# Optimization experiments

Measured on AMD Instinct MI355X. Metric: run time of the kernel, lower is better.

The kernel has to match this reference:

```python
import jax, jax.numpy as jnp
import numpy as np
import math

B, T, C = 4, 2048, 1024
NH = 16
HD = C // NH


def setup_inputs() -> dict:
    key = jax.random.key(0)
    ks = jax.random.split(key, 10)
    s = 0.02
    x = jax.random.normal(ks[0], (B, T, C), dtype=jnp.float32)
    W_qkv = jax.random.normal(ks[1], (C, 3 * C), dtype=jnp.float32) * s
    b_qkv = jnp.zeros((3 * C,), dtype=jnp.float32)
    W_proj = jax.random.normal(ks[2], (C, C), dtype=jnp.float32) * s
    b_proj = jnp.zeros((C,), dtype=jnp.float32)
    asym_mean, asym_std = 1.0, 0.7
    q_scale = jax.random.normal(ks[3], (NH, HD), dtype=jnp.float32) * asym_std + asym_mean
    q_bias = jax.random.normal(ks[4], (NH, HD), dtype=jnp.float32) * asym_std + asym_mean
    k_scale = jax.random.normal(ks[5], (NH, HD), dtype=jnp.float32) * asym_std + asym_mean
    k_bias = jax.random.normal(ks[6], (NH, HD), dtype=jnp.float32) * asym_std + asym_mean
    return {"x": x, "W_qkv": W_qkv, "b_qkv": b_qkv, "W_proj": W_proj,
            "b_proj": b_proj, "q_scale": q_scale, "q_bias": q_bias,
            "k_scale": k_scale, "k_bias": k_bias}


def reference(x, W_qkv, b_qkv, W_proj, b_proj, q_scale, q_bias, k_scale, k_bias):
    Bx, Tx, Cx = x.shape
    qkv = x @ W_qkv + b_qkv                       # [B,T,3C]
    q, k, v = jnp.split(qkv, 3, axis=-1)
    # [B,T,C] -> [B,NH,T,HD]
    reshape = lambda t: t.reshape(Bx, Tx, NH, HD).transpose(0, 2, 1, 3)
    q, k, v = reshape(q), reshape(k), reshape(v)
    # per-head affine scaling of Q/K
    q = q * q_scale[None, :, None, :] + q_bias[None, :, None, :]
    k = k * k_scale[None, :, None, :] + k_bias[None, :, None, :]
    scores = jnp.einsum('bhqd,bhkd->bhqk', q, k) / math.sqrt(HD)  # [B,NH,T,T]
    causal = jnp.tril(jnp.ones((Tx, Tx), dtype=bool))
    scores = jnp.where(causal[None, None], scores, -jnp.inf)
    att = jax.nn.softmax(scores, axis=-1)
    y = jnp.einsum('bhqk,bhkd->bhqd', att, v)     # [B,NH,T,HD]
    y = y.transpose(0, 2, 1, 3).reshape(Bx, Tx, Cx)
    return y @ W_proj + b_proj
```

## Files before the change

kernel.cpp:

```cpp
#include <hip/hip_runtime.h>
#include <hip/hip_bf16.h>

typedef unsigned short u16;
typedef __attribute__((ext_vector_type(8))) short short8;
typedef __attribute__((ext_vector_type(4))) float floatx4;

#define B_SZ 4
#define T_SZ 2048
#define C_SZ 1024
#define NH_SZ 16
#define HD_SZ 64
#define M_TOT 8192
#define K_DIM 1024

#define QSCALE 0.1803368801111204f

#define OFF_XB   ((size_t)16)
#define OFF_WQT  (OFF_XB + 8388608)
#define OFF_WPT  (OFF_WQT + 3145728)
#define OFF_PB   (OFF_WPT + 1048576)
#define OFF_Q    (OFF_PB + 8192)
#define OFF_K    (OFF_Q + 8388608)
#define OFF_V    (OFF_K + 8388608)
#define OFF_Y    (OFF_V + 8388608)
#define PB_BQKV  0
#define PB_BPROJ 3072
#define PB_QSC   4096
#define PB_QBI   5120
#define PB_KSC   6144
#define PB_KBI   7168

__device__ __forceinline__ float bf2f(u16 u) {
    return __uint_as_float(((unsigned)u) << 16);
}
__device__ __forceinline__ u16 f2bf(float f) {
    unsigned x = __float_as_uint(f);
    unsigned r = (x + 0x7fffu + ((x >> 16) & 1u)) >> 16;
    return (u16)r;
}
__device__ __forceinline__ u16 f2bf_fast(float f) {
    return (u16)((__float_as_uint(f) + 0x8000u) >> 16);
}
__device__ __forceinline__ void gl_lds16(const u16* g, u16* l) {
    __builtin_amdgcn_global_load_lds(
        (const __attribute__((address_space(1))) void*)g,
        (__attribute__((address_space(3))) void*)l, 16, 0, 0);
}
__device__ __forceinline__ void wait_vm0() {
    __builtin_amdgcn_s_waitcnt(0x0F70);
}

__global__ __launch_bounds__(256) void detect_k(const u16* __restrict__ x,
                                                int* __restrict__ flag) {
    __shared__ int cnt;
    if (threadIdx.x == 0) cnt = 0;
    __syncthreads();
    int bad = 0;
    for (int i = threadIdx.x; i < 512; i += 256) {
        float v = fabsf(bf2f(x[i]));
        if (v > 1024.0f || (v != 0.0f && v < 9.5367431640625e-7f)) bad++;
    }
    atomicAdd(&cnt, bad);
    __syncthreads();
    if (threadIdx.x == 0) flag[0] = (cnt > 16) ? 1 : 0;
}

__global__ __launch_bounds__(256) void prep_k(
        const void* __restrict__ x,
        const void* __restrict__ Wqkv, const void* __restrict__ Wproj,
        const void* __restrict__ bqkv, const void* __restrict__ bproj,
        const void* __restrict__ qsc, const void* __restrict__ qbi,
        const void* __restrict__ ksc, const void* __restrict__ kbi,
        u16* __restrict__ xb, u16* __restrict__ Wt_qkv,
        u16* __restrict__ Wt_proj, u16* __restrict__ pb,
        const int* __restrict__ flag) {
    __shared__ u16 t[32][33];
    const int blk = blockIdx.x;
    const int isf = flag[0];
    if (blk < 8192) {
        const int i = blk * 256 + threadIdx.x;
        if (isf) {
            const float4 v = ((const float4*)x)[i];
            ushort4 o;
            o.x = f2bf(v.x); o.y = f2bf(v.y); o.z = f2bf(v.z); o.w = f2bf(v.w);
            ((ushort4*)xb)[i] = o;
        } else {
            ((ushort4*)xb)[i] = ((const ushort4*)x)[i];
        }
        return;
    }
    if (blk < 8200) {
        const int i4 = (blk - 8192) * 256 + threadIdx.x;
        if (i4 >= 2048) return;
        const int e = i4 * 4;
        const void* src; int off;
        if (e < 3072)      { src = bqkv;  off = e; }
        else if (e < 4096) { src = bproj; off = e - 3072; }
        else if (e < 5120) { src = qsc;   off = e - 4096; }
        else if (e < 6144) { src = qbi;   off = e - 5120; }
        else if (e < 7168) { src = ksc;   off = e - 6144; }
        else               { src = kbi;   off = e - 7168; }
        ushort4 o;
        if (isf) {
            const float4 v = *(const float4*)((const float*)src + off);
            o.x = f2bf(v.x); o.y = f2bf(v.y); o.z = f2bf(v.z); o.w = f2bf(v.w);
        } else {
            o = *(const ushort4*)((const u16*)src + off);
        }
        *(ushort4*)&pb[e] = o;
        return;
    }
    const void* in; u16* out; int R, C, idx;
    if (blk < 11272) { idx = blk - 8200;  in = Wqkv;  out = Wt_qkv;  R = 1024; C = 3072; }
    else             { idx = blk - 11272; in = Wproj; out = Wt_proj; R = 1024; C = 1024; }
    const int nbx = C >> 5;
    const int c0 = (idx % nbx) * 32, r0 = (idx / nbx) * 32;
    const int tx = threadIdx.x & 31, ty = threadIdx.x >> 5;
    for (int i = 0; i < 4; i++) {
        int r = ty + i * 8;
        size_t gi = (size_t)(r0 + r) * C + c0 + tx;
        t[r][tx] = isf ? f2bf(((const float*)in)[gi]) : ((const u16*)in)[gi];
    }
    __syncthreads();
    for (int i = 0; i < 4; i++) {
        int cr = ty + i * 8;
        out[(size_t)(c0 + cr) * R + r0 + tx] = t[tx][cr];
    }
}

__global__ __launch_bounds__(256) void qkv_gemm(
        const u16* __restrict__ X, const u16* __restrict__ Wt,
        const u16* __restrict__ pb,
        u16* __restrict__ Qb, u16* __restrict__ Kb, u16* __restrict__ Vb) {
    __shared__ __align__(16) u16 As[2][128 * 64];
    __shared__ __align__(16) u16 Bs[2][128 * 64];
    const int bm = blockIdx.y * 128, bn = blockIdx.x * 128;
    const int tid = threadIdx.x;
    const int lane = tid & 63, wave = tid >> 6;
    const int quad = lane >> 4, l16 = lane & 15;
    const int wm = (wave & 1) * 64, wn = (wave >> 1) * 64;
    const int lrow = lane >> 3;
    const int lcol = ((lane & 7) ^ lrow) * 8;

    const u16* xrow = &X[(size_t)(bm + wave * 32 + lrow) * K_DIM + lcol];
    const u16* wrow = &Wt[(size_t)(bn + wave * 32 + lrow) * K_DIM + lcol];

    floatx4 acc[4][4];
    for (int mi = 0; mi < 4; mi++)
        for (int ni = 0; ni < 4; ni++) acc[mi][ni] = 0.f;

    for (int j = 0; j < 4; j++) {
        gl_lds16(xrow + (size_t)j * 8 * K_DIM, &As[0][(wave * 32 + j * 8) * 64]);
        gl_lds16(wrow + (size_t)j * 8 * K_DIM, &Bs[0][(wave * 32 + j * 8) * 64]);
    }

    int cur = 0;
    for (int k0 = 0; k0 < K_DIM; k0 += 64) {
        wait_vm0();
        __syncthreads();
        if (k0 + 64 < K_DIM) {
            const int nb = cur ^ 1;
            for (int j = 0; j < 4; j++) {
                gl_lds16(xrow + (size_t)j * 8 * K_DIM + k0 + 64,
                         &As[nb][(wave * 32 + j * 8) * 64]);
                gl_lds16(wrow + (size_t)j * 8 * K_DIM + k0 + 64,
                         &Bs[nb][(wave * 32 + j * 8) * 64]);
            }
        }
        for (int kk = 0; kk < 64; kk += 32) {
            const int cb = kk >> 3;
            const int slot = ((cb + quad) ^ (l16 & 7)) * 8;
            short8 a[4], b[4];
            for (int mi = 0; mi < 4; mi++)
                a[mi] = *(const short8*)&As[cur][(wm + mi * 16 + l16) * 64 + slot];
            for (int ni = 0; ni < 4; ni++)
                b[ni] = *(const short8*)&Bs[cur][(wn + ni * 16 + l16) * 64 + slot];
            for (int mi = 0; mi < 4; mi++)
                for (int ni = 0; ni < 4; ni++)
                    acc[mi][ni] = __builtin_amdgcn_mfma_f32_16x16x32_bf16(
                        a[mi], b[ni], acc[mi][ni], 0, 0, 0);
        }
        cur ^= 1;
    }

    const int sec = bn >> 10;
    const int bb = bm >> 11;
    const int tbase = bm & 2047;
    for (int mi = 0; mi < 4; mi++) {
        for (int ni = 0; ni < 4; ni++) {
            const int col = bn + wn + ni * 16 + l16;
            const int cmod = col & 1023;
            const int h = cmod >> 6, d = cmod & 63;
            const float bv = bf2f(pb[PB_BQKV + col]);
            if (sec == 2) {
                const int t0 = tbase + wm + mi * 16 + quad * 4;
                ushort4 pk;
                pk.x = f2bf(acc[mi][ni][0] + bv);
                pk.y = f2bf(acc[mi][ni][1] + bv);
                pk.z = f2bf(acc[mi][ni][2] + bv);
                pk.w = f2bf(acc[mi][ni][3] + bv);
                *(ushort4*)&Vb[(((size_t)(bb * NH_SZ + h)) * HD_SZ + d) * T_SZ + t0] = pk;
            } else {
                float sA, sB;
                if (sec == 0) {
                    sA = bf2f(pb[PB_QSC + h * 64 + d]) * QSCALE;
                    sB = bf2f(pb[PB_QBI + h * 64 + d]) * QSCALE;
                } else {
                    sA = bf2f(pb[PB_KSC + h * 64 + d]);
                    sB = bf2f(pb[PB_KBI + h * 64 + d]);
                }
                u16* dstbuf = (sec == 0) ? Qb : Kb;
                for (int r = 0; r < 4; r++) {
                    const int t = tbase + wm + mi * 16 + quad * 4 + r;
                    float v = (acc[mi][ni][r] + bv) * sA + sB;
                    dstbuf[(((size_t)(bb * NH_SZ + h)) * T_SZ + t) * HD_SZ + d] = f2bf(v);
                }
            }
        }
    }
}

__global__ __launch_bounds__(512) void attn_k(const u16* __restrict__ Qb,
                                              const u16* __restrict__ Kb,
                                              const u16* __restrict__ Vtg,
                                              u16* __restrict__ Y) {
    __shared__ __align__(16) u16 Ks[64 * 64];
    __shared__ __align__(16) u16 Vs[64 * 64];
    __shared__ __align__(16) u16 Ps[8 * 16 * 88];
    const int blk = blockIdx.x;
    const int head = blk & 63;
    const int p = blk >> 6;
    const int b = head >> 4, h = head & 15;
    const int tid = threadIdx.x, lane = tid & 63, w = tid >> 6;
    const int quad = lane >> 4, l16 = lane & 15;
    const size_t qk_off = (size_t)head * (T_SZ * HD_SZ);
    const size_t v_off = (size_t)head * (HD_SZ * T_SZ);
    u16* psw = &Ps[w * 1408];
    const int lr = lane >> 3;
    const int lc = ((lane & 7) ^ lr) * 8;
    const int sl0 = ((quad) ^ (l16 & 7)) * 8;
    const int sl1 = ((4 + quad) ^ (l16 & 7)) * 8;

    short8 ones;
    for (int j = 0; j < 8; j++) ones[j] = (short)0x3F80;

    for (int tile = 0; tile < 2; tile++) {
        const int qt = tile ? p : (15 - p);
        const int q0 = qt * 128;
        const int rbase = q0 + w * 16;
        const int q = rbase + l16;

        const short8 aq0 = *(const short8*)&Qb[qk_off + (size_t)q * HD_SZ + quad * 8];
        const short8 aq1 = *(const short8*)&Qb[qk_off + (size_t)q * HD_SZ + 32 + quad * 8];

        floatx4 o[4];
        for (int mi = 0; mi < 4; mi++) o[mi] = 0.f;
        float m_run = -1e30f, l_run = 0.f;

        for (int k0 = 0; k0 < q0 + 128; k0 += 64) {
            __syncthreads();
            gl_lds16(&Kb[qk_off + (size_t)(k0 + w * 8 + lr) * HD_SZ + lc], &Ks[w * 512]);
            gl_lds16(&Vtg[v_off + (size_t)(w * 8 + lr) * T_SZ + k0 + lc], &Vs[w * 512]);
            __syncthreads();
            if (k0 > rbase + 15) continue;

            floatx4 s[4];
            for (int ni = 0; ni < 4; ni++) s[ni] = 0.f;
            for (int ni = 0; ni < 4; ni++)
                s[ni] = __builtin_amdgcn_mfma_f32_16x16x32_bf16(
                    *(const short8*)&Ks[(ni * 16 + l16) * 64 + sl0], aq0, s[ni], 0, 0, 0);
            for (int ni = 0; ni < 4; ni++)
                s[ni] = __builtin_amdgcn_mfma_f32_16x16x32_bf16(
                    *(const short8*)&Ks[(ni * 16 + l16) * 64 + sl1], aq1, s[ni], 0, 0, 0);

            if (k0 + 63 > rbase) {
                for (int ni = 0; ni < 4; ni++)
                    for (int r = 0; r < 4; r++) {
                        int key = k0 + ni * 16 + quad * 4 + r;
                        if (key > q) s[ni][r] = -1e30f;
                    }
            }

            float mx = fmaxf(fmaxf(s[0][0], s[0][1]), fmaxf(s[0][2], s[0][3]));
            for (int ni = 1; ni < 4; ni++)
                mx = fmaxf(mx, fmaxf(fmaxf(s[ni][0], s[ni][1]),
                                     fmaxf(s[ni][2], s[ni][3])));
            mx = fmaxf(mx, __shfl_xor(mx, 16, 64));
            mx = fmaxf(mx, __shfl_xor(mx, 32, 64));
            const float mnew = fmaxf(m_run, mx);
            const float alpha = exp2f(m_run - mnew);
            for (int ni = 0; ni < 4; ni++)
                for (int r = 0; r < 4; r++)
                    s[ni][r] = exp2f(s[ni][r] - mnew);
            m_run = mnew;
            for (int mi = 0; mi < 4; mi++) o[mi] *= alpha;

            for (int ni = 0; ni < 4; ni++) {
                ushort4 pk;
                pk.x = f2bf_fast(s[ni][0]); pk.y = f2bf_fast(s[ni][1]);
                pk.z = f2bf_fast(s[ni][2]); pk.w = f2bf_fast(s[ni][3]);
                *(ushort4*)&psw[l16 * 88 + ni * 16 + quad * 4] = pk;
            }

            floatx4 s4 = 0.f;
            for (int kk = 0; kk < 64; kk += 32) {
                short8 pfr = *(const short8*)&psw[l16 * 88 + kk + quad * 8];
                const int vsl = (kk == 0) ? sl0 : sl1;
                s4 = __builtin_amdgcn_mfma_f32_16x16x32_bf16(ones, pfr, s4, 0, 0, 0);
                for (int mi = 0; mi < 4; mi++) {
                    short8 vfr = *(const short8*)&Vs[(mi * 16 + l16) * 64 + vsl];
                    o[mi] = __builtin_amdgcn_mfma_f32_16x16x32_bf16(vfr, pfr, o[mi], 0, 0, 0);
                }
            }
            l_run = l_run * alpha + s4[0];
        }

        const float inv = 1.0f / l_run;
        u16* yrow = &Y[(((size_t)b * T_SZ + q) * NH_SZ + h) * HD_SZ];
        for (int mi = 0; mi < 4; mi++) {
            ushort4 pk;
            pk.x = f2bf_fast(o[mi][0] * inv); pk.y = f2bf_fast(o[mi][1] * inv);
            pk.z = f2bf_fast(o[mi][2] * inv); pk.w = f2bf_fast(o[mi][3] * inv);
            *(ushort4*)&yrow[mi * 16 + quad * 4] = pk;
        }
    }
}

__global__ __launch_bounds__(256) void proj_gemm(const u16* __restrict__ Yin,
                                                 const u16* __restrict__ Wt,
                                                 const u16* __restrict__ pb,
                                                 void* __restrict__ out,
                                                 const int* __restrict__ flag) {
    __shared__ __align__(16) u16 As[2][128 * 64];
    __shared__ __align__(16) u16 Bs[2][128 * 64];
    const int isf = flag[0];
    const int bm = blockIdx.y * 128, bn = blockIdx.x * 128;
    const int tid = threadIdx.x;
    const int lane = tid & 63, wave = tid >> 6;
    const int quad = lane >> 4, l16 = lane & 15;
    const int wm = (wave & 1) * 64, wn = (wave >> 1) * 64;
    const int lrow = lane >> 3;
    const int lcol = ((lane & 7) ^ lrow) * 8;

    const u16* yrow = &Yin[(size_t)(bm + wave * 32 + lrow) * K_DIM + lcol];
    const u16* wrow = &Wt[(size_t)(bn + wave * 32 + lrow) * K_DIM + lcol];

    floatx4 acc[4][4];
    for (int mi = 0; mi < 4; mi++)
        for (int ni = 0; ni < 4; ni++) acc[mi][ni] = 0.f;

    for (int j = 0; j < 4; j++) {
        gl_lds16(yrow + (size_t)j * 8 * K_DIM, &As[0][(wave * 32 + j * 8) * 64]);
        gl_lds16(wrow + (size_t)j * 8 * K_DIM, &Bs[0][(wave * 32 + j * 8) * 64]);
    }

    int cur = 0;
    for (int k0 = 0; k0 < K_DIM; k0 += 64) {
        wait_vm0();
        __syncthreads();
        if (k0 + 64 < K_DIM) {
            const int nb = cur ^ 1;
            for (int j = 0; j < 4; j++) {
                gl_lds16(yrow + (size_t)j * 8 * K_DIM + k0 + 64,
                         &As[nb][(wave * 32 + j * 8) * 64]);
                gl_lds16(wrow + (size_t)j * 8 * K_DIM + k0 + 64,
                         &Bs[nb][(wave * 32 + j * 8) * 64]);
            }
        }
        for (int kk = 0; kk < 64; kk += 32) {
            const int cb = kk >> 3;
            const int slot = ((cb + quad) ^ (l16 & 7)) * 8;
            short8 a[4], b[4];
            for (int mi = 0; mi < 4; mi++)
                a[mi] = *(const short8*)&As[cur][(wm + mi * 16 + l16) * 64 + slot];
            for (int ni = 0; ni < 4; ni++)
                b[ni] = *(const short8*)&Bs[cur][(wn + ni * 16 + l16) * 64 + slot];
            for (int mi = 0; mi < 4; mi++)
                for (int ni = 0; ni < 4; ni++)
                    acc[mi][ni] = __builtin_amdgcn_mfma_f32_16x16x32_bf16(
                        a[mi], b[ni], acc[mi][ni], 0, 0, 0);
        }
        cur ^= 1;
    }

    for (int mi = 0; mi < 4; mi++) {
        for (int ni = 0; ni < 4; ni++) {
            const int col = bn + wn + ni * 16 + l16;
            const float bv = bf2f(pb[PB_BPROJ + col]);
            for (int r = 0; r < 4; r++) {
                const int row = bm + wm + mi * 16 + quad * 4 + r;
                const float v = acc[mi][ni][r] + bv;
                if (isf) ((float*)out)[(size_t)row * C_SZ + col] = v;
                else     ((u16*)out)[(size_t)row * C_SZ + col] = f2bf(v);
            }
        }
    }
}

extern "C" void kernel_launch(void* const* d_in, const int* in_sizes, int n_in,
                              void* d_out, int out_size, void* d_ws, size_t ws_size,
                              hipStream_t stream) {
    const void* x     = d_in[0];
    const void* Wqkv  = d_in[1];
    const void* bqkv  = d_in[2];
    const void* Wproj = d_in[3];
    const void* bproj = d_in[4];
    const void* qsc   = d_in[5];
    const void* qbi   = d_in[6];
    const void* ksc   = d_in[7];
    const void* kbi   = d_in[8];

    u16* ws = (u16*)d_ws;
    int* flag    = (int*)d_ws;
    u16* xb      = ws + OFF_XB;
    u16* Wt_qkv  = ws + OFF_WQT;
    u16* Wt_proj = ws + OFF_WPT;
    u16* pb      = ws + OFF_PB;
    u16* Qb      = ws + OFF_Q;
    u16* Kb      = ws + OFF_K;
    u16* Vb      = ws + OFF_V;
    u16* Yb      = ws + OFF_Y;

    detect_k<<<1, 256, 0, stream>>>((const u16*)x, flag);
    prep_k<<<12296, 256, 0, stream>>>(x, Wqkv, Wproj, bqkv, bproj,
                                      qsc, qbi, ksc, kbi,
                                      xb, Wt_qkv, Wt_proj, pb, flag);
    qkv_gemm<<<dim3(24, 64), 256, 0, stream>>>(xb, Wt_qkv, pb, Qb, Kb, Vb);
    attn_k<<<dim3(512), 512, 0, stream>>>(Qb, Kb, Vb, Yb);
    proj_gemm<<<dim3(8, 64), 256, 0, stream>>>(Yb, Wt_proj, pb, d_out, flag);
}
```

Before: 323.9 us.

## Single-buffer GEMM staging and fuse both causal query tiles in one attention pass

The QKV and projection GEMMs drop double-buffered async LDS prefetch and go back to a single buffer with load-then-sync, which halves their shared memory footprint. The attention kernel now processes its two paired query tiles (15-p and p) in one sweep over K/V, so each K/V tile is loaded once and shared by both instead of being reloaded for the second tile. It also adds a per-tile P buffer and a min-blocks launch bound. The cost is more registers and LDS in attention, and the GEMMs can no longer hide load latency behind compute.

```diff
diff --git a/kernel.cpp b/kernel.cpp
--- a/kernel.cpp
+++ b/kernel.cpp
@@ -45,9 +45,6 @@
     __builtin_amdgcn_global_load_lds(
         (const __attribute__((address_space(1))) void*)g,
         (__attribute__((address_space(3))) void*)l, 16, 0, 0);
-}
-__device__ __forceinline__ void wait_vm0() {
-    __builtin_amdgcn_s_waitcnt(0x0F70);
 }
 
 __global__ __launch_bounds__(256) void detect_k(const u16* __restrict__ x,
@@ -132,8 +129,8 @@
         const u16* __restrict__ X, const u16* __restrict__ Wt,
         const u16* __restrict__ pb,
         u16* __restrict__ Qb, u16* __restrict__ Kb, u16* __restrict__ Vb) {
-    __shared__ __align__(16) u16 As[2][128 * 64];
-    __shared__ __align__(16) u16 Bs[2][128 * 64];
+    __shared__ __align__(16) u16 As[128 * 64];
+    __shared__ __align__(16) u16 Bs[128 * 64];
     const int bm = blockIdx.y * 128, bn = blockIdx.x * 128;
     const int tid = threadIdx.x;
     const int lane = tid & 63, wave = tid >> 6;
@@ -142,45 +139,31 @@
     const int lrow = lane >> 3;
     const int lcol = ((lane & 7) ^ lrow) * 8;
 
-    const u16* xrow = &X[(size_t)(bm + wave * 32 + lrow) * K_DIM + lcol];
-    const u16* wrow = &Wt[(size_t)(bn + wave * 32 + lrow) * K_DIM + lcol];
-
     floatx4 acc[4][4];
     for (int mi = 0; mi < 4; mi++)
         for (int ni = 0; ni < 4; ni++) acc[mi][ni] = 0.f;
 
-    for (int j = 0; j < 4; j++) {
-        gl_lds16(xrow + (size_t)j * 8 * K_DIM, &As[0][(wave * 32 + j * 8) * 64]);
-        gl_lds16(wrow + (size_t)j * 8 * K_DIM, &Bs[0][(wave * 32 + j * 8) * 64]);
-    }
-
-    int cur = 0;
     for (int k0 = 0; k0 < K_DIM; k0 += 64) {
-        wait_vm0();
-        __syncthreads();
-        if (k0 + 64 < K_DIM) {
-            const int nb = cur ^ 1;
-            for (int j = 0; j < 4; j++) {
-                gl_lds16(xrow + (size_t)j * 8 * K_DIM + k0 + 64,
-                         &As[nb][(wave * 32 + j * 8) * 64]);
-                gl_lds16(wrow + (size_t)j * 8 * K_DIM + k0 + 64,
-                         &Bs[nb][(wave * 32 + j * 8) * 64]);
-            }
-        }
+        __syncthreads();
+        for (int j = 0; j < 4; j++) {
+            const int rb = wave * 32 + j * 8;
+            gl_lds16(&X[(size_t)(bm + rb + lrow) * K_DIM + k0 + lcol], &As[rb * 64]);
+            gl_lds16(&Wt[(size_t)(bn + rb + lrow) * K_DIM + k0 + lcol], &Bs[rb * 64]);
+        }
+        __syncthreads();
         for (int kk = 0; kk < 64; kk += 32) {
             const int cb = kk >> 3;
             const int slot = ((cb + quad) ^ (l16 & 7)) * 8;
             short8 a[4], b[4];
             for (int mi = 0; mi < 4; mi++)
-                a[mi] = *(const short8*)&As[cur][(wm + mi * 16 + l16) * 64 + slot];
+                a[mi] = *(const short8*)&As[(wm + mi * 16 + l16) * 64 + slot];
             for (int ni = 0; ni < 4; ni++)
-                b[ni] = *(const short8*)&Bs[cur][(wn + ni * 16 + l16) * 64 + slot];
+                b[ni] = *(const short8*)&Bs[(wn + ni * 16 + l16) * 64 + slot];
             for (int mi = 0; mi < 4; mi++)
                 for (int ni = 0; ni < 4; ni++)
                     acc[mi][ni] = __builtin_amdgcn_mfma_f32_16x16x32_bf16(
                         a[mi], b[ni], acc[mi][ni], 0, 0, 0);
         }
-        cur ^= 1;
     }
 
     const int sec = bn >> 10;
@@ -220,13 +203,13 @@
     }
 }
 
-__global__ __launch_bounds__(512) void attn_k(const u16* __restrict__ Qb,
-                                              const u16* __restrict__ Kb,
-                                              const u16* __restrict__ Vtg,
-                                              u16* __restrict__ Y) {
+__global__ __launch_bounds__(512, 4) void attn_k(const u16* __restrict__ Qb,
+                                                 const u16* __restrict__ Kb,
+                                                 const u16* __restrict__ Vtg,
+                                                 u16* __restrict__ Y) {
     __shared__ __align__(16) u16 Ks[64 * 64];
     __shared__ __align__(16) u16 Vs[64 * 64];
-    __shared__ __align__(16) u16 Ps[8 * 16 * 88];
+    __shared__ __align__(16) u16 Ps[2 * 8 * 16 * 88];
     const int blk = blockIdx.x;
     const int head = blk & 63;
     const int p = blk >> 6;
@@ -235,7 +218,8 @@
     const int quad = lane >> 4, l16 = lane & 15;
     const size_t qk_off = (size_t)head * (T_SZ * HD_SZ);
     const size_t v_off = (size_t)head * (HD_SZ * T_SZ);
-    u16* psw = &Ps[w * 1408];
+    u16* pswA = &Ps[w * 1408];
+    u16* pswB = &Ps[11264 + w * 1408];
     const int lr = lane >> 3;
     const int lc = ((lane & 7) ^ lr) * 8;
     const int sl0 = ((quad) ^ (l16 & 7)) * 8;
@@ -244,83 +228,135 @@
     short8 ones;
     for (int j = 0; j < 8; j++) ones[j] = (short)0x3F80;
 
-    for (int tile = 0; tile < 2; tile++) {
-        const int qt = tile ? p : (15 - p);
-        const int q0 = qt * 128;
-        const int rbase = q0 + w * 16;
-        const int q = rbase + l16;
-
-        const short8 aq0 = *(const short8*)&Qb[qk_off + (size_t)q * HD_SZ + quad * 8];
-        const short8 aq1 = *(const short8*)&Qb[qk_off + (size_t)q * HD_SZ + 32 + quad * 8];
-
-        floatx4 o[4];
-        for (int mi = 0; mi < 4; mi++) o[mi] = 0.f;
-        float m_run = -1e30f, l_run = 0.f;
-
-        for (int k0 = 0; k0 < q0 + 128; k0 += 64) {
-            __syncthreads();
-            gl_lds16(&Kb[qk_off + (size_t)(k0 + w * 8 + lr) * HD_SZ + lc], &Ks[w * 512]);
-            gl_lds16(&Vtg[v_off + (size_t)(w * 8 + lr) * T_SZ + k0 + lc], &Vs[w * 512]);
-            __syncthreads();
-            if (k0 > rbase + 15) continue;
-
-            floatx4 s[4];
-            for (int ni = 0; ni < 4; ni++) s[ni] = 0.f;
-            for (int ni = 0; ni < 4; ni++)
-                s[ni] = __builtin_amdgcn_mfma_f32_16x16x32_bf16(
-                    *(const short8*)&Ks[(ni * 16 + l16) * 64 + sl0], aq0, s[ni], 0, 0, 0);
-            for (int ni = 0; ni < 4; ni++)
-                s[ni] = __builtin_amdgcn_mfma_f32_16x16x32_bf16(
-                    *(const short8*)&Ks[(ni * 16 + l16) * 64 + sl1], aq1, s[ni], 0, 0, 0);
-
-            if (k0 + 63 > rbase) {
+    const int rbA = (15 - p) * 128 + w * 16, qA = rbA + l16;
+    const int rbB = p * 128 + w * 16,        qB = rbB + l16;
+
+    const short8 aqA0 = *(const short8*)&Qb[qk_off + (size_t)qA * HD_SZ + quad * 8];
+    const short8 aqA1 = *(const short8*)&Qb[qk_off + (size_t)qA * HD_SZ + 32 + quad * 8];
+    const short8 aqB0 = *(const short8*)&Qb[qk_off + (size_t)qB * HD_SZ + quad * 8];
+    const short8 aqB1 = *(const short8*)&Qb[qk_off + (size_t)qB * HD_SZ + 32 + quad * 8];
+
+    floatx4 oA[4], oB[4];
+    for (int mi = 0; mi < 4; mi++) { oA[mi] = 0.f; oB[mi] = 0.f; }
+    float mA = -1e30f, lA = 0.f, mB = -1e30f, lB = 0.f;
+
+    const int kend = (16 - p) * 128;
+    for (int k0 = 0; k0 < kend; k0 += 64) {
+        __syncthreads();
+        gl_lds16(&Kb[qk_off + (size_t)(k0 + w * 8 + lr) * HD_SZ + lc], &Ks[w * 512]);
+        gl_lds16(&Vtg[v_off + (size_t)(w * 8 + lr) * T_SZ + k0 + lc], &Vs[w * 512]);
+        __syncthreads();
+        const bool doA = (k0 <= rbA + 15);
+        const bool doB = (k0 <= rbB + 15);
+        if (!doA && !doB) continue;
+
+        floatx4 sA[4], sB[4];
+        if (doA) for (int ni = 0; ni < 4; ni++) sA[ni] = 0.f;
+        if (doB) for (int ni = 0; ni < 4; ni++) sB[ni] = 0.f;
+        for (int ni = 0; ni < 4; ni++) {
+            const short8 kf = *(const short8*)&Ks[(ni * 16 + l16) * 64 + sl0];
+            if (doA) sA[ni] = __builtin_amdgcn_mfma_f32_16x16x32_bf16(kf, aqA0, sA[ni], 0, 0, 0);
+            if (doB) sB[ni] = __builtin_amdgcn_mfma_f32_16x16x32_bf16(kf, aqB0, sB[ni], 0, 0, 0);
+        }
+        for (int ni = 0; ni < 4; ni++) {
+            const short8 kf = *(const short8*)&Ks[(ni * 16 + l16) * 64 + sl1];
+            if (doA) sA[ni] = __builtin_amdgcn_mfma_f32_16x16x32_bf16(kf, aqA1, sA[ni], 0, 0, 0);
+            if (doB) sB[ni] = __builtin_amdgcn_mfma_f32_16x16x32_bf16(kf, aqB1, sB[ni], 0, 0, 0);
+        }
+
+        float alphaA = 1.f, alphaB = 1.f;
+        if (doA) {
+            if (k0 + 63 > rbA)
                 for (int ni = 0; ni < 4; ni++)
                     for (int r = 0; r < 4; r++) {
                         int key = k0 + ni * 16 + quad * 4 + r;
-                        if (key > q) s[ni][r] = -1e30f;
+                        if (key > qA) sA[ni][r] = -1e30f;
                     }
-            }
-
-            float mx = fmaxf(fmaxf(s[0][0], s[0][1]), fmaxf(s[0][2], s[0][3]));
+            float mx = fmaxf(fmaxf(sA[0][0], sA[0][1]), fmaxf(sA[0][2], sA[0][3]));
             for (int ni = 1; ni < 4; ni++)
-                mx = fmaxf(mx, fmaxf(fmaxf(s[ni][0], s[ni][1]),
-                                     fmaxf(s[ni][2], s[ni][3])));
+                mx = fmaxf(mx, fmaxf(fmaxf(sA[ni][0], sA[ni][1]),
+                                     fmaxf(sA[ni][2], sA[ni][3])));
             mx = fmaxf(mx, __shfl_xor(mx, 16, 64));
             mx = fmaxf(mx, __shfl_xor(mx, 32, 64));
-            const float mnew = fmaxf(m_run, mx);
-            const float alpha = exp2f(m_run - mnew);
+            const float mnew = fmaxf(mA, mx);
+            alphaA = exp2f(mA - mnew);
             for (int ni = 0; ni < 4; ni++)
-                for (int r = 0; r < 4; r++)
-                    s[ni][r] = exp2f(s[ni][r] - mnew);
-            m_run = mnew;
-            for (int mi = 0; mi < 4; mi++) o[mi] *= alpha;
-
+                for (int r = 0; r < 4; r++) sA[ni][r] = exp2f(sA[ni][r] - mnew);
+            mA = mnew;
+            for (int mi = 0; mi < 4; mi++) oA[mi] *= alphaA;
             for (int ni = 0; ni < 4; ni++) {
                 ushort4 pk;
-                pk.x = f2bf_fast(s[ni][0]); pk.y = f2bf_fast(s[ni][1]);
-                pk.z = f2bf_fast(s[ni][2]); pk.w = f2bf_fast(s[ni][3]);
-                *(ushort4*)&psw[l16 * 88 + ni * 16 + quad * 4] = pk;
-            }
-
-            floatx4 s4 = 0.f;
-            for (int kk = 0; kk < 64; kk += 32) {
-                short8 pfr = *(const short8*)&psw[l16 * 88 + kk + quad * 8];
-                const int vsl = (kk == 0) ? sl0 : sl1;
-                s4 = __builtin_amdgcn_mfma_f32_16x16x32_bf16(ones, pfr, s4, 0, 0, 0);
-                for (int mi = 0; mi < 4; mi++) {
-                    short8 vfr = *(const short8*)&Vs[(mi * 16 + l16) * 64 + vsl];
-                    o[mi] = __builtin_amdgcn_mfma_f32_16x16x32_bf16(vfr, pfr, o[mi], 0, 0, 0);
-                }
-            }
-            l_run = l_run * alpha + s4[0];
-        }
-
-        const float inv = 1.0f / l_run;
-        u16* yrow = &Y[(((size_t)b * T_SZ + q) * NH_SZ + h) * HD_SZ];
+                pk.x = f2bf_fast(sA[ni][0]); pk.y = f2bf_fast(sA[ni][1]);
+                pk.z = f2bf_fast(sA[ni][2]); pk.w = f2bf_fast(sA[ni][3]);
+                *(ushort4*)&pswA[l16 * 88 + ni * 16 + quad * 4] = pk;
+            }
+        }
+        if (doB) {
+            if (k0 + 63 > rbB)
+                for (int ni = 0; ni < 4; ni++)
+                    for (int r = 0; r < 4; r++) {
+                        int key = k0 + ni * 16 + quad * 4 + r;
+                        if (key > qB) sB[ni][r] = -1e30f;
+                    }
+            float mx = fmaxf(fmaxf(sB[0][0], sB[0][1]), fmaxf(sB[0][2], sB[0][3]));
+            for (int ni = 1; ni < 4; ni++)
+                mx = fmaxf(mx, fmaxf(fmaxf(sB[ni][0], sB[ni][1]),
+                                     fmaxf(sB[ni][2], sB[ni][3])));
+            mx = fmaxf(mx, __shfl_xor(mx, 16, 64));
+            mx = fmaxf(mx, __shfl_xor(mx, 32, 64));
+            const float mnew = fmaxf(mB, mx);
+            alphaB = exp2f(mB - mnew);
+            for (int ni = 0; ni < 4; ni++)
+                for (int r = 0; r < 4; r++) sB[ni][r] = exp2f(sB[ni][r] - mnew);
+            mB = mnew;
+            for (int mi = 0; mi < 4; mi++) oB[mi] *= alphaB;
+            for (int ni = 0; ni < 4; ni++) {
+                ushort4 pk;
+                pk.x = f2bf_fast(sB[ni][0]); pk.y = f2bf_fast(sB[ni][1]);
+                pk.z = f2bf_fast(sB[ni][2]); pk.w = f2bf_fast(sB[ni][3]);
+                *(ushort4*)&pswB[l16 * 88 + ni * 16 + quad * 4] = pk;
+            }
+        }
+
+        floatx4 s4A = 0.f, s4B = 0.f;
+        for (int kk = 0; kk < 64; kk += 32) {
+            const int vsl = (kk == 0) ? sl0 : sl1;
+            short8 pfrA, pfrB;
+            if (doA) {
+                pfrA = *(const short8*)&pswA[l16 * 88 + kk + quad * 8];
+                s4A = __builtin_amdgcn_mfma_f32_16x16x32_bf16(ones, pfrA, s4A, 0, 0, 0);
+            }
+            if (doB) {
+                pfrB = *(const short8*)&pswB[l16 * 88 + kk + quad * 8];
+                s4B = __builtin_amdgcn_mfma_f32_16x16x32_bf16(ones, pfrB, s4B, 0, 0, 0);
+            }
+            for (int mi = 0; mi < 4; mi++) {
+                const short8 vf = *(const short8*)&Vs[(mi * 16 + l16) * 64 + vsl];
+                if (doA) oA[mi] = __builtin_amdgcn_mfma_f32_16x16x32_bf16(vf, pfrA, oA[mi], 0, 0, 0);
+                if (doB) oB[mi] = __builtin_amdgcn_mfma_f32_16x16x32_bf16(vf, pfrB, oB[mi], 0, 0, 0);
+            }
+        }
+        if (doA) lA = lA * alphaA + s4A[0];
+        if (doB) lB = lB * alphaB + s4B[0];
+    }
+
+    {
+        const float inv = 1.0f / lA;
+        u16* yrow = &Y[(((size_t)b * T_SZ + qA) * NH_SZ + h) * HD_SZ];
         for (int mi = 0; mi < 4; mi++) {
             ushort4 pk;
-            pk.x = f2bf_fast(o[mi][0] * inv); pk.y = f2bf_fast(o[mi][1] * inv);
-            pk.z = f2bf_fast(o[mi][2] * inv); pk.w = f2bf_fast(o[mi][3] * inv);
+            pk.x = f2bf_fast(oA[mi][0] * inv); pk.y = f2bf_fast(oA[mi][1] * inv);
+            pk.z = f2bf_fast(oA[mi][2] * inv); pk.w = f2bf_fast(oA[mi][3] * inv);
+            *(ushort4*)&yrow[mi * 16 + quad * 4] = pk;
+        }
+    }
+    {
+        const float inv = 1.0f / lB;
+        u16* yrow = &Y[(((size_t)b * T_SZ + qB) * NH_SZ + h) * HD_SZ];
+        for (int mi = 0; mi < 4; mi++) {
+            ushort4 pk;
+            pk.x = f2bf_fast(oB[mi][0] * inv); pk.y = f2bf_fast(oB[mi][1] * inv);
+            pk.z = f2bf_fast(oB[mi][2] * inv); pk.w = f2bf_fast(oB[mi][3] * inv);
             *(ushort4*)&yrow[mi * 16 + quad * 4] = pk;
         }
     }
@@ -331,8 +367,8 @@
                                                  const u16* __restrict__ pb,
                                                  void* __restrict__ out,
                                                  const int* __restrict__ flag) {
-    __shared__ __align__(16) u16 As[2][128 * 64];
-    __shared__ __align__(16) u16 Bs[2][128 * 64];
+    __shared__ __align__(16) u16 As[128 * 64];
+    __shared__ __align__(16) u16 Bs[128 * 64];
     const int isf = flag[0];
     const int bm = blockIdx.y * 128, bn = blockIdx.x * 128;
     const int tid = threadIdx.x;
@@ -342,45 +378,31 @@
     const int lrow = lane >> 3;
     const int lcol = ((lane & 7) ^ lrow) * 8;
 
-    const u16* yrow = &Yin[(size_t)(bm + wave * 32 + lrow) * K_DIM + lcol];
-    const u16* wrow = &Wt[(size_t)(bn + wave * 32 + lrow) * K_DIM + lcol];
-
     floatx4 acc[4][4];
     for (int mi = 0; mi < 4; mi++)
         for (int ni = 0; ni < 4; ni++) acc[mi][ni] = 0.f;
 
-    for (int j = 0; j < 4; j++) {
-        gl_lds16(yrow + (size_t)j * 8 * K_DIM, &As[0][(wave * 32 + j * 8) * 64]);
-        gl_lds16(wrow + (size_t)j * 8 * K_DIM, &Bs[0][(wave * 32 + j * 8) * 64]);
-    }
-
-    int cur = 0;
     for (int k0 = 0; k0 < K_DIM; k0 += 64) {
-        wait_vm0();
-        __syncthreads();
-        if (k0 + 64 < K_DIM) {
-            const int nb = cur ^ 1;
-            for (int j = 0; j < 4; j++) {
-                gl_lds16(yrow + (size_t)j * 8 * K_DIM + k0 + 64,
-                         &As[nb][(wave * 32 + j * 8) * 64]);
-                gl_lds16(wrow + (size_t)j * 8 * K_DIM + k0 + 64,
-                         &Bs[nb][(wave * 32 + j * 8) * 64]);
-            }
-        }
+        __syncthreads();
+        for (int j = 0; j < 4; j++) {
+            const int rb = wave * 32 + j * 8;
+            gl_lds16(&Yin[(size_t)(bm + rb + lrow) * K_DIM + k0 + lcol], &As[rb * 64]);
+            gl_lds16(&Wt[(size_t)(bn + rb + lrow) * K_DIM + k0 + lcol], &Bs[rb * 64]);
+        }
+        __syncthreads();
         for (int kk = 0; kk < 64; kk += 32) {
             const int cb = kk >> 3;
             const int slot = ((cb + quad) ^ (l16 & 7)) * 8;
             short8 a[4], b[4];
             for (int mi = 0; mi < 4; mi++)
-                a[mi] = *(const short8*)&As[cur][(wm + mi * 16 + l16) * 64 + slot];
+                a[mi] = *(const short8*)&As[(wm + mi * 16 + l16) * 64 + slot];
             for (int ni = 0; ni < 4; ni++)
-                b[ni] = *(const short8*)&Bs[cur][(wn + ni * 16 + l16) * 64 + slot];
+                b[ni] = *(const short8*)&Bs[(wn + ni * 16 + l16) * 64 + slot];
             for (int mi = 0; mi < 4; mi++)
                 for (int ni = 0; ni < 4; ni++)
                     acc[mi][ni] = __builtin_amdgcn_mfma_f32_16x16x32_bf16(
                         a[mi], b[ni], acc[mi][ni], 0, 0, 0);
         }
-        cur ^= 1;
     }
 
     for (int mi = 0; mi < 4; mi++) {
```

Result: slower. 771.9 us (+138.3%).
